# Performance work log

Measured on AMD Instinct MI355X. Metric: run time of the kernel, lower is better.

The kernel has to match this reference:

```python
import jax, jax.numpy as jnp
import numpy as np


def setup_inputs() -> dict:
    key = jax.random.key(0)
    k1, k2, k3 = jax.random.split(key, 3)
    B, N, C, K = 4, 8192, 256, 16
    q = jax.random.normal(k1, (B, N, C), dtype=jnp.float32)
    q_pos = jax.random.normal(k2, (B, N, 3), dtype=jnp.float32)
    W = jax.random.normal(k3, (2 * C, C), dtype=jnp.float32) / np.sqrt(2 * C)
    b = jnp.zeros((C,), dtype=jnp.float32)
    return {"q": q, "q_pos": q_pos, "W": W, "b": b, "k": K}


def _square_distance(src, dst):
    # src [B,N,3], dst [B,M,3] -> [B,N,M]
    d = -2.0 * jnp.einsum("bnc,bmc->bnm", src, dst)
    d = d + jnp.sum(src * src, axis=-1)[:, :, None]
    d = d + jnp.sum(dst * dst, axis=-1)[:, None, :]
    return d


def reference(q, q_pos, W, b, k):
    # self-attention path: v = q, v_pos = q_pos
    v, v_pos = q, q_pos
    sqrdists = _square_distance(q_pos, v_pos)           # [B,N,M]
    _, idx = jax.lax.top_k(-sqrdists, k)                # k smallest -> [B,N,k]
    # gather neighbors: local_v[b,n,j] = v[b, idx[b,n,j]]
    local_v = jax.vmap(lambda vv, ii: vv[ii])(v, idx)   # [B,N,k,C]
    qk = jnp.broadcast_to(q[:, :, None, :], local_v.shape)
    feature = jnp.concatenate([local_v - qk, qk], axis=-1)  # [B,N,k,2C]
    h = jnp.einsum("bnkf,fc->bnkc", feature, W) + b
    h = jax.nn.leaky_relu(h, negative_slope=0.2)
    out = jnp.max(h, axis=-2)                           # [B,N,C]
    return out
```

## Files before the change

kernel.cpp:

```cpp
#include <hip/hip_runtime.h>
#include <hip/hip_bf16.h>
#include <cstdint>
#include <cstddef>

#define BATCH 4
#define NPT   8192
#define CH    256
#define KNN   16
#define BN_TOT (BATCH * NPT)
#define NSLICE 16
#define SLICE  (NPT / NSLICE)
#define CAP    32

typedef __attribute__((ext_vector_type(8))) short bf16x8;
typedef __attribute__((ext_vector_type(4))) float f32x4;

__device__ __forceinline__ float dist2np(const float4 qp, const float4 cp) {
#pragma clang fp contract(off)
  float acc = qp.x * cp.x;
  acc = __builtin_fmaf(qp.y, cp.y, acc);
  acc = __builtin_fmaf(qp.z, cp.z, acc);
  float t = -2.0f * acc;
  t = t + qp.w;
  t = t + cp.w;
  return t;
}

__device__ __forceinline__ unsigned int pk_bf16(float a, float b) {
  __hip_bfloat162 h = __float22bfloat162_rn(make_float2(a, b));
  return *(unsigned int*)&h;
}

__global__ __launch_bounds__(256) void prep_kernel(
    const float* __restrict__ q_pos, const float* __restrict__ W,
    float4* __restrict__ cpack, unsigned short* __restrict__ WbT)
{
  int t = blockIdx.x * 256 + threadIdx.x;
  {
    int k = t >> 9;
    int j = t & 511;
    float v;
    if (j < 256) {
      v = W[k * 256 + j];
    } else {
      int c = j - 256;
      v = W[(256 + k) * 256 + c] - W[k * 256 + c];
    }
    __hip_bfloat16 hb = __float2bfloat16(v);
    WbT[(size_t)j * 256 + k] = *(unsigned short*)&hb;
  }
  if (t < BN_TOT) {
#pragma clang fp contract(off)
    float x = q_pos[3 * t + 0];
    float y = q_pos[3 * t + 1];
    float z = q_pos[3 * t + 2];
    float px = x * x;
    float py = y * y;
    float pz = z * z;
    float s = px + py;
    s = s + pz;
    cpack[t] = make_float4(x, y, z, s);
  }
}

__global__ __launch_bounds__(1024, 8) void knn_kernel(
    const float4* __restrict__ cpack,
    int* __restrict__ idxout)
{
  __shared__ unsigned short cand[NSLICE * 64 * CAP];
  __shared__ unsigned int hist[32][64];
  __shared__ unsigned short scnt[NSLICE][64];
  __shared__ float edge_s[64];

  const int tid = threadIdx.x;
  const int l   = tid & 63;
  const int w   = __builtin_amdgcn_readfirstlane(tid >> 6);
  const int b   = blockIdx.y;
  const int q   = b * NPT + blockIdx.x * 64 + l;

  ((unsigned int*)hist)[tid] = 0u;
  ((unsigned int*)hist)[tid + 1024] = 0u;
  __syncthreads();

  const float4 qp = cpack[q];
  const float m2x = -2.0f * qp.x, m2y = -2.0f * qp.y, m2z = -2.0f * qp.z;
  const float4* __restrict__ cb = cpack + b * NPT;
  const int m0 = w * SLICE;
  unsigned int* hl = &hist[0][l];

#pragma unroll 4
  for (int m = m0; m < m0 + SLICE; ++m) {
    float4 cp = cb[m];
    float d = fmaf(m2z, cp.z, fmaf(m2y, cp.y, fmaf(m2x, cp.x, qp.w + cp.w)));
    int e = (__float_as_int(d) >> 22) - 241;
    int bin = min(max(e, 0), 31);
    atomicAdd(hl + (bin << 6), 1u);
  }
  __syncthreads();

  if (tid < 64) {
    int cum = 0, B = 31;
#pragma unroll 1
    for (int bb = 0; bb < 32; ++bb) {
      cum += (int)hist[bb][tid];
      if (cum >= KNN) { B = bb; break; }
    }
    edge_s[tid] = __uint_as_float((unsigned)(242 + B) << 22);
  }
  __syncthreads();

  const float edgef = edge_s[l];
  unsigned int cnt = 0;
  unsigned short* mybuf = &cand[(w * 64 + l) * CAP];
#pragma unroll 2
  for (int m = m0; m < m0 + SLICE; ++m) {
    float4 cp = cb[m];
    float d = fmaf(m2z, cp.z, fmaf(m2y, cp.y, fmaf(m2x, cp.x, qp.w + cp.w)));
    if (d < edgef) {
      if (cnt < CAP) mybuf[cnt] = (unsigned short)m;
      cnt++;
    }
  }
  scnt[w][l] = (unsigned short)(cnt < (unsigned)CAP ? cnt : (unsigned)CAP);
  __syncthreads();

  if (tid < 64) {
    int (*outs)[17] = (int(*)[17])hist;
    const int nself = (q & (NPT - 1));
#pragma unroll
    for (int j = 0; j < 16; ++j) outs[l][j] = nself;

    float r[16];
#pragma unroll
    for (int i = 0; i < 16; ++i) r[i] = __builtin_inff();
#pragma unroll 1
    for (int w2 = 0; w2 < NSLICE; ++w2) {
      int cw = (int)scnt[w2][l];
      for (int i = 0; i < cw; ++i) {
        int m = (int)cand[(w2 * 64 + l) * CAP + i];
        float d = dist2np(qp, cb[m]);
        if (d < r[15]) {
          float prev = -__builtin_inff();
#pragma unroll
          for (int j = 0; j < 16; ++j) {
            float rj = r[j];
            r[j] = fminf(fmaxf(prev, d), rj);
            prev = rj;
          }
        }
      }
    }
    const float T = r[15];

    int front = 0, tie_i = 0;
#pragma unroll 1
    for (int w2 = 0; w2 < NSLICE; ++w2) {
      int cw = (int)scnt[w2][l];
      for (int i = 0; i < cw; ++i) {
        int m = (int)cand[(w2 * 64 + l) * CAP + i];
        float d = dist2np(qp, cb[m]);
        if (d < T) {
          outs[l][front] = m;
          front++;
        } else if (d == T) {
          int pos = 15 - tie_i;
          if (pos >= front) outs[l][pos] = m;
          tie_i++;
        }
      }
    }
#pragma unroll
    for (int j = 0; j < 16; ++j) idxout[(size_t)q * 16 + j] = outs[l][j];
  }
}

#define ASTRIDE 40
__global__ __launch_bounds__(256) void gemm_kernel(
    const float* __restrict__ Q, const unsigned short* __restrict__ WbT,
    const float* __restrict__ bias,
    unsigned short* __restrict__ A16, float* __restrict__ Qn)
{
  __shared__ __align__(16) unsigned short As[128 * ASTRIDE];
  __shared__ __align__(16) unsigned short Bs[128 * ASTRIDE];
  const int tid  = threadIdx.x;
  const int lane = tid & 63;
  const int wv   = tid >> 6;
  const int wr   = wv & 1, wc = wv >> 1;
  const int bm0  = blockIdx.x * 128;
  const int bn0  = blockIdx.y * 128;
  const int srow = tid >> 1;
  const int skh  = tid & 1;
  const int quad = lane >> 4;
  const int l15  = lane & 15;

  f32x4 acc[4][4];
#pragma unroll
  for (int i = 0; i < 4; ++i)
#pragma unroll
    for (int j = 0; j < 4; ++j) acc[i][j] = (f32x4)0.0f;

  const float* ag = Q + (size_t)(bm0 + srow) * 256 + skh * 16;
  const unsigned short* bg = WbT + (size_t)(bn0 + srow) * 256 + skh * 16;
  unsigned short* asw = &As[srow * ASTRIDE + skh * 16];
  unsigned short* bsw = &Bs[srow * ASTRIDE + skh * 16];

  for (int k0 = 0; k0 < 256; k0 += 32) {
    float4 f0 = *(const float4*)(ag + k0);
    float4 f1 = *(const float4*)(ag + k0 + 4);
    float4 f2 = *(const float4*)(ag + k0 + 8);
    float4 f3 = *(const float4*)(ag + k0 + 12);
    uint4 bv0 = *(const uint4*)(bg + k0);
    uint4 bv1 = *(const uint4*)(bg + k0 + 8);
    uint4 a0, a1;
    a0.x = pk_bf16(f0.x, f0.y); a0.y = pk_bf16(f0.z, f0.w);
    a0.z = pk_bf16(f1.x, f1.y); a0.w = pk_bf16(f1.z, f1.w);
    a1.x = pk_bf16(f2.x, f2.y); a1.y = pk_bf16(f2.z, f2.w);
    a1.z = pk_bf16(f3.x, f3.y); a1.w = pk_bf16(f3.z, f3.w);
    __syncthreads();
    *(uint4*)(asw) = a0;
    *(uint4*)(asw + 8) = a1;
    *(uint4*)(bsw) = bv0;
    *(uint4*)(bsw + 8) = bv1;
    __syncthreads();

    bf16x8 af[4], bf[4];
#pragma unroll
    for (int rt = 0; rt < 4; ++rt)
      af[rt] = *(const bf16x8*)&As[(wr * 64 + rt * 16 + l15) * ASTRIDE + quad * 8];
#pragma unroll
    for (int ct = 0; ct < 4; ++ct)
      bf[ct] = *(const bf16x8*)&Bs[(wc * 64 + ct * 16 + l15) * ASTRIDE + quad * 8];
#pragma unroll
    for (int rt = 0; rt < 4; ++rt)
#pragma unroll
      for (int ct = 0; ct < 4; ++ct)
        acc[rt][ct] = __builtin_amdgcn_mfma_f32_16x16x32_bf16(af[rt], bf[ct], acc[rt][ct], 0, 0, 0);
  }

  if (bn0 < 256) {
#pragma unroll
    for (int ct = 0; ct < 4; ++ct) {
      int col = bn0 + wc * 64 + ct * 16 + l15;
#pragma unroll
      for (int rt = 0; rt < 4; ++rt) {
        int rowb = bm0 + wr * 64 + rt * 16 + quad * 4;
#pragma unroll
        for (int r = 0; r < 4; ++r) {
          __hip_bfloat16 hb = __float2bfloat16(acc[rt][ct][r]);
          A16[(size_t)(rowb + r) * 256 + col] = *(unsigned short*)&hb;
        }
      }
    }
  } else {
#pragma unroll
    for (int ct = 0; ct < 4; ++ct) {
      int col = bn0 + wc * 64 + ct * 16 + l15 - 256;
      float bvl = bias[col];
#pragma unroll
      for (int rt = 0; rt < 4; ++rt) {
        int rowb = bm0 + wr * 64 + rt * 16 + quad * 4;
#pragma unroll
        for (int r = 0; r < 4; ++r)
          Qn[(size_t)(rowb + r) * 256 + col] = acc[rt][ct][r] + bvl;
      }
    }
  }
}

__global__ __launch_bounds__(256) void gather_kernel(
    const unsigned short* __restrict__ A16, const int* __restrict__ idxout,
    float* __restrict__ Out)
{
  __shared__ int sidx[16];
  const int q = blockIdx.x;
  const int b = q >> 13;
  const int c = threadIdx.x;
  if (c < 16) sidx[c] = idxout[(size_t)q * 16 + c];
  __syncthreads();
  const float qn = Out[(size_t)q * 256 + c];
  const unsigned short* __restrict__ Ab = A16 + (size_t)b * NPT * 256;
  float best = -__builtin_inff();
#pragma unroll
  for (int j = 0; j < 16; ++j) {
    unsigned short raw = Ab[(size_t)sidx[j] * 256 + c];
    float a = __uint_as_float((unsigned)raw << 16);
    float h = a + qn;
    best = fmaxf(best, fmaxf(h, 0.2f * h));
  }
  Out[(size_t)q * 256 + c] = best;
}

extern "C" void kernel_launch(void* const* d_in, const int* in_sizes, int n_in,
                              void* d_out, int out_size, void* d_ws, size_t ws_size,
                              hipStream_t stream)
{
  (void)in_sizes; (void)n_in; (void)out_size; (void)ws_size;
  const float* qf   = (const float*)d_in[0];
  const float* qpos = (const float*)d_in[1];
  const float* W    = (const float*)d_in[2];
  const float* bias = (const float*)d_in[3];

  char* ws = (char*)d_ws;
  size_t off = 0;
  auto alloc = [&](size_t bytes) {
    void* p = ws + off;
    off += (bytes + 255) & ~(size_t)255;
    return p;
  };
  float4* cpack       = (float4*)alloc((size_t)BN_TOT * sizeof(float4));
  unsigned short* WbT = (unsigned short*)alloc((size_t)512 * 256 * 2);
  int* idxout         = (int*)alloc((size_t)BN_TOT * KNN * sizeof(int));
  unsigned short* A16 = (unsigned short*)alloc((size_t)BN_TOT * CH * 2);
  float* Out          = (float*)d_out;

  prep_kernel<<<512, 256, 0, stream>>>(qpos, W, cpack, WbT);
  knn_kernel<<<dim3(128, BATCH), 1024, 0, stream>>>(cpack, idxout);
  gemm_kernel<<<dim3(256, 4), 256, 0, stream>>>(qf, WbT, bias, A16, Out);
  gather_kernel<<<BN_TOT, 256, 0, stream>>>(A16, idxout, Out);
}
```

Baseline: 308.5 us.

## Skip far-bin histogram atomics and parallelize kNN selection across four waves

The histogram pass now first bins a small prefix of each slice, derives a per-query upper bin bound, and skips atomic increments for candidates beyond that bound. The final top-16 selection is split across four waves, each keeping a sorted distance/index list over four slices. A single wave then does a 4-way merge from shared memory, which replaces the old two-pass threshold-then-collect scan. This cuts LDS atomics and serial work in the tail, at the cost of more shared-memory traffic and a merge step whose tie ordering may differ from the reference.

```diff
diff --git a/kernel.cpp b/kernel.cpp
--- a/kernel.cpp
+++ b/kernel.cpp
@@ -11,6 +11,7 @@
 #define NSLICE 16
 #define SLICE  (NPT / NSLICE)
 #define CAP    32
+#define MINI   32
 
 typedef __attribute__((ext_vector_type(8))) short bf16x8;
 typedef __attribute__((ext_vector_type(4))) float f32x4;
@@ -67,10 +68,11 @@
     const float4* __restrict__ cpack,
     int* __restrict__ idxout)
 {
-  __shared__ unsigned short cand[NSLICE * 64 * CAP];
+  __shared__ __align__(16) unsigned short cand[NSLICE * 64 * CAP];
   __shared__ unsigned int hist[32][64];
   __shared__ unsigned short scnt[NSLICE][64];
   __shared__ float edge_s[64];
+  __shared__ int ubnd[64];
 
   const int tid = threadIdx.x;
   const int l   = tid & 63;
@@ -86,15 +88,37 @@
   const float m2x = -2.0f * qp.x, m2y = -2.0f * qp.y, m2z = -2.0f * qp.z;
   const float4* __restrict__ cb = cpack + b * NPT;
   const int m0 = w * SLICE;
-  unsigned int* hl = &hist[0][l];
+  unsigned int* hb = (unsigned int*)((char*)&hist[0][0] - (241 << 8)) + l;
 
 #pragma unroll 4
-  for (int m = m0; m < m0 + SLICE; ++m) {
+  for (int m = m0; m < m0 + MINI; ++m) {
     float4 cp = cb[m];
     float d = fmaf(m2z, cp.z, fmaf(m2y, cp.y, fmaf(m2x, cp.x, qp.w + cp.w)));
-    int e = (__float_as_int(d) >> 22) - 241;
-    int bin = min(max(e, 0), 31);
-    atomicAdd(hl + (bin << 6), 1u);
+    int r = __float_as_int(d) >> 22;
+    r = min(max(r, 241), 272);
+    atomicAdd(hb + (r << 6), 1u);
+  }
+  __syncthreads();
+
+  if (tid < 64) {
+    int cum = 0, Bm = 31;
+#pragma unroll 1
+    for (int bb = 0; bb < 32; ++bb) {
+      cum += (int)hist[bb][tid];
+      if (cum >= KNN) { Bm = bb; break; }
+    }
+    ubnd[tid] = 241 + Bm;
+  }
+  __syncthreads();
+
+  const int ub = ubnd[l];
+#pragma unroll 4
+  for (int m = m0 + MINI; m < m0 + SLICE; ++m) {
+    float4 cp = cb[m];
+    float d = fmaf(m2z, cp.z, fmaf(m2y, cp.y, fmaf(m2x, cp.x, qp.w + cp.w)));
+    int r = __float_as_int(d) >> 22;
+    r = min(max(r, 241), 272);
+    if (r <= ub) atomicAdd(hb + (r << 6), 1u);
   }
   __syncthreads();
 
@@ -124,53 +148,66 @@
   scnt[w][l] = (unsigned short)(cnt < (unsigned)CAP ? cnt : (unsigned)CAP);
   __syncthreads();
 
-  if (tid < 64) {
-    int (*outs)[17] = (int(*)[17])hist;
+  if ((tid >> 6) < 4) {
+    const int g = tid >> 6;
     const int nself = (q & (NPT - 1));
-#pragma unroll
-    for (int j = 0; j < 16; ++j) outs[l][j] = nself;
-
-    float r[16];
-#pragma unroll
-    for (int i = 0; i < 16; ++i) r[i] = __builtin_inff();
+    float rd[16]; int ri[16];
+#pragma unroll
+    for (int j = 0; j < 16; ++j) { rd[j] = __builtin_inff(); ri[j] = nself; }
 #pragma unroll 1
-    for (int w2 = 0; w2 < NSLICE; ++w2) {
+    for (int w2 = 4 * g; w2 < 4 * g + 4; ++w2) {
       int cw = (int)scnt[w2][l];
       for (int i = 0; i < cw; ++i) {
         int m = (int)cand[(w2 * 64 + l) * CAP + i];
         float d = dist2np(qp, cb[m]);
-        if (d < r[15]) {
-          float prev = -__builtin_inff();
-#pragma unroll
-          for (int j = 0; j < 16; ++j) {
-            float rj = r[j];
-            r[j] = fminf(fmaxf(prev, d), rj);
-            prev = rj;
+        if (d < rd[15]) {
+#pragma unroll
+          for (int j = 15; j > 0; --j) {
+            bool up = d < rd[j - 1];
+            float nd = up ? rd[j - 1] : d;
+            int   ni = up ? ri[j - 1] : m;
+            if (d < rd[j]) { rd[j] = nd; ri[j] = ni; }
           }
+          if (d < rd[0]) { rd[0] = d; ri[0] = m; }
         }
       }
     }
-    const float T = r[15];
-
-    int front = 0, tie_i = 0;
+    float2* pls = (float2*)(cand + (size_t)g * 8192);
+#pragma unroll
+    for (int j = 0; j < 16; ++j) {
+      int pos = (j + l) & 15;
+      pls[l * 16 + pos] = make_float2(rd[j], __int_as_float(ri[j]));
+    }
+  }
+  __syncthreads();
+
+  if (tid < 64) {
+    const float2* pls0 = (const float2*)(cand);
+    const float2* pls1 = (const float2*)(cand + 8192);
+    const float2* pls2 = (const float2*)(cand + 16384);
+    const float2* pls3 = (const float2*)(cand + 24576);
+    int p0 = 0, p1 = 0, p2 = 0, p3 = 0;
+    float2 h0 = pls0[l * 16 + (l & 15)];
+    float2 h1 = pls1[l * 16 + (l & 15)];
+    float2 h2 = pls2[l * 16 + (l & 15)];
+    float2 h3 = pls3[l * 16 + (l & 15)];
 #pragma unroll 1
-    for (int w2 = 0; w2 < NSLICE; ++w2) {
-      int cw = (int)scnt[w2][l];
-      for (int i = 0; i < cw; ++i) {
-        int m = (int)cand[(w2 * 64 + l) * CAP + i];
-        float d = dist2np(qp, cb[m]);
-        if (d < T) {
-          outs[l][front] = m;
-          front++;
-        } else if (d == T) {
-          int pos = 15 - tie_i;
-          if (pos >= front) outs[l][pos] = m;
-          tie_i++;
-        }
-      }
-    }
-#pragma unroll
-    for (int j = 0; j < 16; ++j) idxout[(size_t)q * 16 + j] = outs[l][j];
+    for (int s = 0; s < 16; ++s) {
+      float bd = h0.x; int be = __float_as_int(h0.y); int bg = 0;
+      if (h1.x < bd) { bd = h1.x; be = __float_as_int(h1.y); bg = 1; }
+      if (h2.x < bd) { bd = h2.x; be = __float_as_int(h2.y); bg = 2; }
+      if (h3.x < bd) { bd = h3.x; be = __float_as_int(h3.y); bg = 3; }
+      idxout[(size_t)q * 16 + s] = be;
+      p0 += (bg == 0); p1 += (bg == 1); p2 += (bg == 2); p3 += (bg == 3);
+      int q0 = p0 < 16 ? p0 : 15;
+      int q1 = p1 < 16 ? p1 : 15;
+      int q2 = p2 < 16 ? p2 : 15;
+      int q3 = p3 < 16 ? p3 : 15;
+      h0 = pls0[l * 16 + ((q0 + l) & 15)];
+      h1 = pls1[l * 16 + ((q1 + l) & 15)];
+      h2 = pls2[l * 16 + ((q2 + l) & 15)];
+      h3 = pls3[l * 16 + ((q3 + l) & 15)];
+    }
   }
 }
 
```

Result: faster. 290.0 us (-6.0%).
